# Optimization experiments

Measured on AMD Instinct MI355X. Metric: run time of the kernel, lower is better.

The kernel has to match this reference:

```python
import jax, jax.numpy as jnp
import numpy as np


def setup_inputs() -> dict:
    key = jax.random.key(0)
    k1, k2 = jax.random.split(key)
    z = jax.random.normal(k1, (16, 256, 4096), dtype=jnp.float32)  # (B, z_dim, T)
    embedding = jax.random.normal(k2, (1024, 256), dtype=jnp.float32)  # (z_num, z_dim)
    return {"z": z, "embedding": embedding}


def reference(z, embedding):
    # z: (B, C, T) -> (B, T, C), matching z.transpose(1, 2)
    zt = jnp.transpose(z, (0, 2, 1))
    B, T, C = zt.shape
    z_flat = zt.reshape(-1, C)  # (N, C), N = B*T

    # squared-euclidean distances: ||z||^2 + ||e||^2 - 2 z e^T  -> (N, K)
    distances = (
        jnp.sum(z_flat * z_flat, axis=1, keepdims=True)
        + jnp.sum(embedding * embedding, axis=1)
        - 2.0 * z_flat @ embedding.T
    )
    encoding_idx = jnp.argmin(distances, axis=1)  # (N,)
    z_vq = embedding[encoding_idx].reshape(B, T, C)

    # perplexity of code usage (one-hot scatter -> mean)
    K = embedding.shape[0]
    counts = jnp.zeros((K,), dtype=jnp.float32).at[encoding_idx].add(1.0)
    avg_probs = counts / encoding_idx.shape[0]
    perplexity = jnp.exp(-jnp.sum(avg_probs * jnp.log(avg_probs + 1e-10)))

    # sparsity = cross_entropy(E E^T, arange) = mean(logsumexp(row) - diag)
    logits = embedding @ embedding.T  # (K, K)
    sparsity = jnp.mean(jax.nn.logsumexp(logits, axis=1) - jnp.diag(logits))

    sg = jax.lax.stop_gradient
    z_qut_loss = jnp.sum((z_vq - sg(zt)) ** 2)   # mse_loss reduction='sum'
    z_enc_loss = jnp.sum((sg(z_vq) - zt) ** 2)

    # straight-through estimator
    z_st = zt + sg(z_vq - zt)
    out = jnp.transpose(z_st, (0, 2, 1))  # back to (B, C, T)
    return (out, z_qut_loss, z_enc_loss, perplexity, sparsity)
```

## Files before the change

### kernel.cpp

```cpp
#include <hip/hip_runtime.h>
#include <math.h>

typedef unsigned int u32;
typedef unsigned long long u64;
typedef _Float16 f16x8 __attribute__((ext_vector_type(8)));
typedef _Float16 f16x4 __attribute__((ext_vector_type(4)));
typedef float f32x4 __attribute__((ext_vector_type(4)));
typedef __attribute__((address_space(1))) const char gch;
typedef __attribute__((address_space(3))) char lch;

#define ZD 256
#define KC 1024
#define TT 4096
#define BB 16
#define NROWS (BB*TT)
#define TAU 0.12f
#define FLAGCAP 32768

__device__ __forceinline__ u32 flip32(float s) {
    int i = __float_as_int(s);
    return (u32)(i ^ ((i >> 31) | 0x80000000));
}
__device__ __forceinline__ float unflip32(u32 u) {
    int m = (~(((int)u) >> 31)) | 0x80000000;
    return __int_as_float((int)(u ^ (u32)m));
}

__global__ __launch_bounds__(256)
void vq_prep_kernel(const float* __restrict__ emb, _Float16* __restrict__ eh,
                    float* __restrict__ re, int* __restrict__ cnt) {
    int gid = blockIdx.x * 256 + threadIdx.x;
    if (gid < 2) cnt[gid] = 0;

    int code = gid >> 6;
    int lane = threadIdx.x & 63;
    float4 v = *(const float4*)(emb + (size_t)code * ZD + lane * 4);
    float s = v.x*v.x + v.y*v.y + v.z*v.z + v.w*v.w;
    #pragma unroll
    for (int off = 32; off; off >>= 1) s += __shfl_down(s, off, 64);
    if (lane == 0) re[code] = s;

    f16x4 hv;
    hv[0] = (_Float16)v.x; hv[1] = (_Float16)v.y;
    hv[2] = (_Float16)v.z; hv[3] = (_Float16)v.w;
    *(f16x4*)(eh + (size_t)code * ZD + lane * 4) = hv;
}

__device__ __forceinline__ void stage_half8(const char* ehc, char* dstbase,
                                            int h, int w, int l) {
    const int srow = h * 16384;
    #pragma unroll
    for (int j = 0; j < 2; ++j) {
        const int gi  = w * 2 + j;
        const int c   = 2 * gi + (l >> 5);
        const int kbs = (l & 31) * 16;
        const int off = srow + c * 512 + (kbs ^ ((c & 7) << 4));
        __builtin_amdgcn_global_load_lds((gch*)(ehc + off),
                                         (lch*)(dstbase + gi * 1024), 16, 0, 0);
    }
}

__device__ __forceinline__ void compute_phase16(const char* hb, int h,
                                                const f16x8 (&ah)[8], const float* reL,
                                                float (&v1)[4], float (&v2)[4], int (&i1)[4],
                                                int lane15, int lk) {
    #pragma unroll
    for (int cg = 0; cg < 2; ++cg) {
        const int c  = cg * 16 + lane15;
        const int sw = (lane15 & 7) << 4;
        f16x8 bh[8];
        #pragma unroll
        for (int ks = 0; ks < 8; ++ks)
            bh[ks] = *(const f16x8*)(hb + c * 512 + ((lk * 16 + ks * 64) ^ sw));

        f32x4 ae = {0.f, 0.f, 0.f, 0.f};
        f32x4 ao = {0.f, 0.f, 0.f, 0.f};
        __builtin_amdgcn_s_setprio(1);
        #pragma unroll
        for (int ks = 0; ks < 4; ++ks) {
            ae = __builtin_amdgcn_mfma_f32_16x16x32_f16(ah[2 * ks],     bh[2 * ks],     ae, 0, 0, 0);
            ao = __builtin_amdgcn_mfma_f32_16x16x32_f16(ah[2 * ks + 1], bh[2 * ks + 1], ao, 0, 0, 0);
        }
        __builtin_amdgcn_s_setprio(0);

        const int codeg = h * 32 + c;
        const float rc = reL[codeg];
        #pragma unroll
        for (int r = 0; r < 4; ++r) {
            float s0 = fmaf(-2.f, ae[r] + ao[r], rc);
            float n2 = fminf(fmaxf(v1[r], s0), v2[r]);
            i1[r] = (s0 < v1[r]) ? codeg : i1[r];
            v1[r] = fminf(v1[r], s0);
            v2[r] = n2;
        }
    }
}

__global__ __launch_bounds__(512, 4)
void vq_argmin_mfma(const float* __restrict__ z, const _Float16* __restrict__ eh,
                    const float* __restrict__ emb, const float* __restrict__ re,
                    float* __restrict__ out, float* __restrict__ lossP,
                    int* __restrict__ idx, int* __restrict__ cnt,
                    int* __restrict__ flags) {
    __shared__ __align__(16) char lds[53248];
    float* reL    = (float*)(lds + 49152);
    int*   idsL   = (int*)lds;
    float* wlossL = (float*)(lds + 1024);

    const int tid = threadIdx.x;
    const int w   = tid >> 6;
    const int l   = tid & 63;
    const int lane15 = l & 15;
    const int lk     = l >> 4;
    const int r0  = blockIdx.x * 128;
    const int b   = r0 >> 12;
    const int t0  = r0 & 4095;
    const char* ehc = (const char*)eh;

    *(float2*)(reL + tid * 2) = *(const float2*)(re + tid * 2);

    f16x8 ah[8];
    float zsq = 0.f;
    {
        const char* zb = (const char*)(z + (size_t)b * ZD * TT + t0 + w * 16);
        char* zdst = lds + w * 4096;
        #pragma unroll
        for (int round = 0; round < 4; ++round) {
            #pragma unroll
            for (int j = 0; j < 4; ++j) {
                const int cl = j * 16 + (l >> 2);
                const int tb = (l & 3) * 16;
                const int c  = round * 64 + cl;
                const char* src = zb + (size_t)c * TT * 4 + tb;
                __builtin_amdgcn_global_load_lds((gch*)src, (lch*)(zdst + j * 1024),
                                                 16, 0, 0);
            }
            asm volatile("s_waitcnt vmcnt(0)" ::: "memory");
            __builtin_amdgcn_sched_barrier(0);
            #pragma unroll
            for (int ks2 = 0; ks2 < 2; ++ks2) {
                const int cl0 = ks2 * 32 + lk * 8;
                f16x8 h;
                #pragma unroll
                for (int j = 0; j < 8; ++j) {
                    float v = *(const float*)(zdst + (cl0 + j) * 64 + lane15 * 4);
                    zsq = fmaf(v, v, zsq);
                    h[j] = (_Float16)v;
                }
                ah[round * 2 + ks2] = h;
            }
            asm volatile("s_waitcnt lgkmcnt(0)" ::: "memory");
            __builtin_amdgcn_sched_barrier(0);
        }
    }
    zsq += __shfl_xor(zsq, 16, 64);
    zsq += __shfl_xor(zsq, 32, 64);

    float v1[4], v2[4];
    int   i1[4];
    #pragma unroll
    for (int r = 0; r < 4; ++r) { v1[r] = 3.4e38f; v2[r] = 3.4e38f; i1[r] = 0; }

    asm volatile("s_waitcnt vmcnt(0) lgkmcnt(0)" ::: "memory");
    __syncthreads();
    stage_half8(ehc, lds,         0, w, l);
    stage_half8(ehc, lds + 16384, 1, w, l);

    for (int h = 0; h < 31; ++h) {
        asm volatile("s_waitcnt vmcnt(2)" ::: "memory");
        __builtin_amdgcn_sched_barrier(0);
        __builtin_amdgcn_s_barrier();
        if (h < 30) stage_half8(ehc, lds + ((h + 2) % 3) * 16384, h + 2, w, l);
        compute_phase16(lds + (h % 3) * 16384, h, ah, reL, v1, v2, i1, lane15, lk);
    }
    asm volatile("s_waitcnt vmcnt(0)" ::: "memory");
    __builtin_amdgcn_sched_barrier(0);
    __builtin_amdgcn_s_barrier();
    compute_phase16(lds + (31 % 3) * 16384, 31, ah, reL, v1, v2, i1, lane15, lk);

    #pragma unroll
    for (int off = 1; off < 16; off <<= 1) {
        #pragma unroll
        for (int r = 0; r < 4; ++r) {
            float ov1 = __shfl_xor(v1[r], off, 64);
            int   oi1 = __shfl_xor(i1[r], off, 64);
            float ov2 = __shfl_xor(v2[r], off, 64);
            float nv2 = fminf(fmaxf(v1[r], ov1), fminf(v2[r], ov2));
            if (ov1 < v1[r] || (ov1 == v1[r] && oi1 < i1[r])) { v1[r] = ov1; i1[r] = oi1; }
            v2[r] = nv2;
        }
    }

    float zsr[4];
    #pragma unroll
    for (int r = 0; r < 4; ++r) zsr[r] = __shfl(zsq, lk * 4 + r, 64);

    __syncthreads();
    float lossw = 0.f;
    if (lane15 == 0) {
        #pragma unroll
        for (int r = 0; r < 4; ++r) {
            const int row = w * 16 + lk * 4 + r;
            idsL[row] = i1[r];
            const bool fl = (v2[r] - v1[r] < TAU);
            lossw += fl ? zsr[r] : (zsr[r] + v1[r]);
            if (fl) {
                int p = atomicAdd(cnt, 1);
                if (p < FLAGCAP) flags[p] = (r0 + row) | (i1[r] << 16);
            }
        }
    }
    lossw += __shfl_xor(lossw, 16, 64);
    lossw += __shfl_xor(lossw, 32, 64);
    if (l == 0) wlossL[w] = lossw;
    __syncthreads();

    if (tid < 128) idx[r0 + tid] = idsL[tid];
    if (tid == 0) {
        float s = 0.f;
        #pragma unroll
        for (int j = 0; j < 8; ++j) s += wlossL[j];
        lossP[blockIdx.x] = s;
    }

    {
        const int c0 = w * 32;
        float* ob = out + (size_t)b * ZD * TT + t0;
        #pragma unroll
        for (int half = 0; half < 2; ++half) {
            const int tt = half * 64 + l;
            const int ii = idsL[tt];
            const float4* er4 = (const float4*)(emb + (size_t)ii * ZD + c0);
            #pragma unroll
            for (int c4 = 0; c4 < 8; ++c4) {
                float4 ev = er4[c4];
                float* o0 = ob + (size_t)(c0 + c4 * 4) * TT + tt;
                o0[0]      = ev.x;
                o0[TT]     = ev.y;
                o0[2 * TT] = ev.z;
                o0[3 * TT] = ev.w;
            }
        }
    }
}

__global__ __launch_bounds__(256)
void vq_fixup_spar(const float* __restrict__ z, const float* __restrict__ emb,
                   const float* __restrict__ re, const int* __restrict__ cnt,
                   const int* __restrict__ flags, float* __restrict__ out,
                   int* __restrict__ idx, float* __restrict__ spar,
                   float* __restrict__ addP) {
    const int tid = threadIdx.x;
    const int w   = tid >> 6;
    const int lane = tid & 63;

    if (blockIdx.x >= 128) {
        __shared__ __align__(16) float er[8][260];
        __shared__ float wmaxS[8][4];
        __shared__ float wsumS[8][4];
        __shared__ float shD[8];
        const int bid2 = blockIdx.x - 128;
        const int r0   = bid2 * 8;

        for (int i = tid; i < 8 * 256; i += 256) er[i >> 8][i & 255] = emb[(size_t)r0 * ZD + i];
        __syncthreads();

        float dots[4][8];
        #pragma unroll
        for (int cc = 0; cc < 4; ++cc) {
            const int c = cc * 256 + tid;
            const float4* ec = (const float4*)(emb + (size_t)c * ZD);
            float a[8] = {0.f,0.f,0.f,0.f,0.f,0.f,0.f,0.f};
            for (int k4 = 0; k4 < ZD / 4; ++k4) {
                float4 e4 = ec[k4];
                #pragma unroll
                for (int r = 0; r < 8; ++r) {
                    const float* a4 = &er[r][k4 * 4];
                    a[r] = fmaf(e4.x, a4[0], fmaf(e4.y, a4[1],
                           fmaf(e4.z, a4[2], fmaf(e4.w, a4[3], a[r]))));
                }
            }
            #pragma unroll
            for (int r = 0; r < 8; ++r) dots[cc][r] = a[r];
            const int gr = c - r0;
            if (gr >= 0 && gr < 8) shD[gr] = a[gr];
        }
        #pragma unroll
        for (int r = 0; r < 8; ++r) {
            float m = fmaxf(fmaxf(dots[0][r], dots[1][r]), fmaxf(dots[2][r], dots[3][r]));
            #pragma unroll
            for (int off = 32; off; off >>= 1) m = fmaxf(m, __shfl_xor(m, off, 64));
            if (lane == 0) wmaxS[r][w] = m;
        }
        __syncthreads();
        #pragma unroll
        for (int r = 0; r < 8; ++r) {
            const float M = fmaxf(fmaxf(wmaxS[r][0], wmaxS[r][1]),
                                  fmaxf(wmaxS[r][2], wmaxS[r][3]));
            float se = expf(dots[0][r] - M) + expf(dots[1][r] - M)
                     + expf(dots[2][r] - M) + expf(dots[3][r] - M);
            #pragma unroll
            for (int off = 32; off; off >>= 1) se += __shfl_xor(se, off, 64);
            if (lane == 0) wsumS[r][w] = se;
        }
        __syncthreads();
        if (tid == 0) {
            float acc = 0.f;
            #pragma unroll
            for (int r = 0; r < 8; ++r) {
                const float M = fmaxf(fmaxf(wmaxS[r][0], wmaxS[r][1]),
                                      fmaxf(wmaxS[r][2], wmaxS[r][3]));
                const float S = wsumS[r][0] + wsumS[r][1] + wsumS[r][2] + wsumS[r][3];
                acc += M + logf(S) - shD[r];
            }
            spar[bid2] = acc;
        }
        return;
    }

    __shared__ __align__(16) float zs[8][ZD];
    __shared__ u64 sb[4][8];
    __shared__ int nwS[8];
    __shared__ float addS;
    int n = cnt[0];
    if (n > FLAGCAP) n = FLAGCAP;
    float blkLoss = 0.f;

    for (int base = blockIdx.x * 8; base < n; base += 128 * 8) {
        const int nr = (n - base < 8) ? (n - base) : 8;
        __syncthreads();
        for (int i = tid; i < nr * 256; i += 256) {
            const int r = i >> 8, k = i & 255;
            const int rowg = flags[base + r] & 0xFFFF;
            zs[r][k] = z[(size_t)(rowg >> 12) * ZD * TT + (size_t)k * TT + (rowg & 4095)];
        }
        __syncthreads();

        u64 best[8];
        #pragma unroll
        for (int r = 0; r < 8; ++r) best[r] = 0xFFFFFFFFFFFFFFFFull;

        for (int cc = 0; cc < 4; ++cc) {
            const int c = cc * 256 + tid;
            const float4* ec = (const float4*)(emb + (size_t)c * ZD);
            float a[8] = {0.f,0.f,0.f,0.f,0.f,0.f,0.f,0.f};
            for (int k4 = 0; k4 < ZD / 4; ++k4) {
                float4 e4 = ec[k4];
                #pragma unroll
                for (int r = 0; r < 8; ++r) {
                    const float* a4 = &zs[r][k4 * 4];
                    a[r] = fmaf(e4.x, a4[0], fmaf(e4.y, a4[1],
                           fmaf(e4.z, a4[2], fmaf(e4.w, a4[3], a[r]))));
                }
            }
            const float rc = re[c];
            #pragma unroll
            for (int r = 0; r < 8; ++r) {
                if (r < nr) {
                    float s = fmaf(-2.f, a[r], rc);
                    u64 pk = ((u64)flip32(s) << 32) | (u32)c;
                    if (pk < best[r]) best[r] = pk;
                }
            }
        }
        #pragma unroll
        for (int r = 0; r < 8; ++r) {
            if (r < nr) {
                u64 bv = best[r];
                #pragma unroll
                for (int off = 32; off; off >>= 1) {
                    u64 o = (u64)__shfl_xor((long long)bv, off, 64);
                    if (o < bv) bv = o;
                }
                if (lane == 0) sb[w][r] = bv;
            }
        }
        __syncthreads();
        if (tid == 0) addS = 0.f;
        __syncthreads();
        if (tid < nr) {
            u64 m = sb[0][tid];
            if (sb[1][tid] < m) m = sb[1][tid];
            if (sb[2][tid] < m) m = sb[2][tid];
            if (sb[3][tid] < m) m = sb[3][tid];
            const int nc  = (int)(u32)(m & 0xFFFFFFFFull);
            const float s = unflip32((u32)(m >> 32));
            const int rowg = flags[base + tid] & 0xFFFF;
            const int old  = (flags[base + tid] >> 16) & 1023;
            atomicAdd(&addS, s);
            if (nc != old) { idx[rowg] = nc; nwS[tid] = nc; }
            else nwS[tid] = -1;
        }
        __syncthreads();
        if (tid == 0) blkLoss += addS;
        for (int r = 0; r < nr; ++r) {
            const int nw = nwS[r];
            if (nw >= 0) {
                const int rowg = flags[base + r] & 0xFFFF;
                out[(size_t)(rowg >> 12) * ZD * TT + (size_t)tid * TT + (rowg & 4095)]
                    = emb[(size_t)nw * ZD + tid];
            }
        }
    }
    if (tid == 0) addP[blockIdx.x] = blkLoss;
}

__global__ __launch_bounds__(1024)
void vq_final_kernel(const int* __restrict__ idx, const float* __restrict__ spar,
                     const float* __restrict__ lossP, const float* __restrict__ addP,
                     float* __restrict__ scal) {
    __shared__ int   histL[4][1024];
    __shared__ float red[1024];
    const int tid = threadIdx.x;
    const int g   = tid >> 8;

    histL[0][tid] = 0; histL[1][tid] = 0; histL[2][tid] = 0; histL[3][tid] = 0;
    __syncthreads();
    #pragma unroll 4
    for (int i = 0; i < 64; ++i)
        atomicAdd(&histL[g][idx[i * 1024 + tid]], 1);
    __syncthreads();
    const int hc = histL[0][tid] + histL[1][tid] + histL[2][tid] + histL[3][tid];
    float p = (float)hc * (1.0f / (float)NROWS);
    red[tid] = -p * logf(p + 1e-10f);
    __syncthreads();
    for (int st = 512; st; st >>= 1) {
        if (tid < st) red[tid] += red[tid + st];
        __syncthreads();
    }
    if (tid == 0) scal[2] = expf(red[0]);
    __syncthreads();

    red[tid] = (tid < 512 ? lossP[tid] : 0.f) + ((tid < 128) ? addP[tid] : 0.f);
    __syncthreads();
    for (int st = 512; st; st >>= 1) {
        if (tid < st) red[tid] += red[tid + st];
        __syncthreads();
    }
    if (tid == 0) { scal[0] = red[0]; scal[1] = red[0]; }
    __syncthreads();

    red[tid] = (tid < 128) ? spar[tid] : 0.f;
    __syncthreads();
    for (int st = 512; st; st >>= 1) {
        if (tid < st) red[tid] += red[tid + st];
        __syncthreads();
    }
    if (tid == 0) scal[3] = red[0] * (1.0f / (float)KC);
}

extern "C" void kernel_launch(void* const* d_in, const int* in_sizes, int n_in,
                              void* d_out, int out_size, void* d_ws, size_t ws_size,
                              hipStream_t stream) {
    const float* z   = (const float*)d_in[0];
    const float* emb = (const float*)d_in[1];
    float* out = (float*)d_out;
    const size_t NOUT = (size_t)BB * ZD * TT;
    float* scal = out + NOUT;

    float* re    = (float*)d_ws;
    int*   cnt   = (int*)(re + KC);
    int*   flags = cnt + 4;
    float* spar  = (float*)(flags + FLAGCAP);
    float* lossP = spar + 128;
    float* addP  = lossP + 512;
    int*   idx   = (int*)(addP + 128);
    _Float16* eh = (_Float16*)(idx + NROWS);

    vq_prep_kernel<<<256, 256, 0, stream>>>(emb, eh, re, cnt);
    vq_argmin_mfma<<<NROWS / 128, 512, 0, stream>>>(z, eh, emb, re, out, lossP, idx,
                                                    cnt, flags);
    vq_fixup_spar<<<256, 256, 0, stream>>>(z, emb, re, cnt, flags, out, idx, spar, addP);
    vq_final_kernel<<<1, 1024, 0, stream>>>(idx, spar, lossP, addP, scal);
}
```

Before: 172.0 us.

## Move sparsity logsumexp blocks into argmin kernel and widen fixup grid

The K×K sparsity logsumexp work moves out of the fixup kernel and into extra blocks appended to the main MFMA argmin launch. Those blocks now run 512 threads over two column chunks, so they overlap with argmin work instead of waiting behind it. The fixup kernel becomes a pure recompute kernel with 256 blocks instead of 128, and its partial-loss buffer is widened to match. The extra blocks share the argmin kernel's launch bounds and LDS footprint, which could affect how blocks are scheduled and distributed.

```diff
diff --git a/kernel.cpp b/kernel.cpp
--- a/kernel.cpp
+++ b/kernel.cpp
@@ -101,13 +101,85 @@
                     const float* __restrict__ emb, const float* __restrict__ re,
                     float* __restrict__ out, float* __restrict__ lossP,
                     int* __restrict__ idx, int* __restrict__ cnt,
-                    int* __restrict__ flags) {
+                    int* __restrict__ flags, float* __restrict__ spar) {
     __shared__ __align__(16) char lds[53248];
+
+    const int tid = threadIdx.x;
+
+    if (blockIdx.x >= 512) {
+        float* er    = (float*)lds;
+        float* wmaxS = (float*)(lds + 8320);
+        float* wsumS = wmaxS + 64;
+        float* shD   = wsumS + 64;
+        const int bid2 = blockIdx.x - 512;
+        const int r0s  = bid2 * 8;
+        const int wv = tid >> 6, lane = tid & 63;
+
+        for (int i = tid; i < 8 * 256; i += 512)
+            er[(i >> 8) * 260 + (i & 255)] = emb[(size_t)r0s * ZD + i];
+        __syncthreads();
+
+        float dots[2][8];
+        #pragma unroll
+        for (int cc = 0; cc < 2; ++cc) {
+            const int c = cc * 512 + tid;
+            const float4* ec = (const float4*)(emb + (size_t)c * ZD);
+            float a[8] = {0.f,0.f,0.f,0.f,0.f,0.f,0.f,0.f};
+            #pragma unroll 4
+            for (int k4 = 0; k4 < ZD / 4; ++k4) {
+                float4 e4 = ec[k4];
+                #pragma unroll
+                for (int r = 0; r < 8; ++r) {
+                    const float* a4 = &er[r * 260 + k4 * 4];
+                    a[r] = fmaf(e4.x, a4[0], fmaf(e4.y, a4[1],
+                           fmaf(e4.z, a4[2], fmaf(e4.w, a4[3], a[r]))));
+                }
+            }
+            #pragma unroll
+            for (int r = 0; r < 8; ++r) dots[cc][r] = a[r];
+            const int gr = c - r0s;
+            if (gr >= 0 && gr < 8) shD[gr] = a[gr];
+        }
+        #pragma unroll
+        for (int r = 0; r < 8; ++r) {
+            float m = fmaxf(dots[0][r], dots[1][r]);
+            #pragma unroll
+            for (int off = 32; off; off >>= 1) m = fmaxf(m, __shfl_xor(m, off, 64));
+            if (lane == 0) wmaxS[r * 8 + wv] = m;
+        }
+        __syncthreads();
+        #pragma unroll
+        for (int r = 0; r < 8; ++r) {
+            float M = wmaxS[r * 8];
+            #pragma unroll
+            for (int j = 1; j < 8; ++j) M = fmaxf(M, wmaxS[r * 8 + j]);
+            float se = expf(dots[0][r] - M) + expf(dots[1][r] - M);
+            #pragma unroll
+            for (int off = 32; off; off >>= 1) se += __shfl_xor(se, off, 64);
+            if (lane == 0) wsumS[r * 8 + wv] = se;
+        }
+        __syncthreads();
+        if (tid == 0) {
+            float acc = 0.f;
+            #pragma unroll
+            for (int r = 0; r < 8; ++r) {
+                float M = wmaxS[r * 8];
+                #pragma unroll
+                for (int j = 1; j < 8; ++j) M = fmaxf(M, wmaxS[r * 8 + j]);
+                float S = 0.f;
+                #pragma unroll
+                for (int j = 0; j < 8; ++j) S += wsumS[r * 8 + j];
+                acc += M + logf(S) - shD[r];
+            }
+            spar[bid2] = acc;
+        }
+        return;
+    }
+
     float* reL    = (float*)(lds + 49152);
     int*   idsL   = (int*)lds;
     float* wlossL = (float*)(lds + 1024);
 
-    const int tid = threadIdx.x;
     const int w   = tid >> 6;
     const int l   = tid & 63;
     const int lane15 = l & 15;
@@ -245,105 +317,40 @@
 }
 
 __global__ __launch_bounds__(256)
-void vq_fixup_spar(const float* __restrict__ z, const float* __restrict__ emb,
-                   const float* __restrict__ re, const int* __restrict__ cnt,
-                   const int* __restrict__ flags, float* __restrict__ out,
-                   int* __restrict__ idx, float* __restrict__ spar,
-                   float* __restrict__ addP) {
+void vq_fixup_kernel(const float* __restrict__ z, const float* __restrict__ emb,
+                     const float* __restrict__ re, const int* __restrict__ cnt,
+                     const int* __restrict__ flags, float* __restrict__ out,
+                     int* __restrict__ idx, float* __restrict__ addP) {
+    __shared__ __align__(16) float zs[8][ZD];
+    __shared__ u64 sb[4][8];
+    __shared__ int nwS[8];
+    __shared__ float addS;
     const int tid = threadIdx.x;
     const int w   = tid >> 6;
     const int lane = tid & 63;
-
-    if (blockIdx.x >= 128) {
-        __shared__ __align__(16) float er[8][260];
-        __shared__ float wmaxS[8][4];
-        __shared__ float wsumS[8][4];
-        __shared__ float shD[8];
-        const int bid2 = blockIdx.x - 128;
-        const int r0   = bid2 * 8;
-
-        for (int i = tid; i < 8 * 256; i += 256) er[i >> 8][i & 255] = emb[(size_t)r0 * ZD + i];
-        __syncthreads();
-
-        float dots[4][8];
-        #pragma unroll
+    int n = cnt[0];
+    if (n > FLAGCAP) n = FLAGCAP;
+    float blkLoss = 0.f;
+
+    for (int base = blockIdx.x * 8; base < n; base += 256 * 8) {
+        const int nr = (n - base < 8) ? (n - base) : 8;
+        __syncthreads();
+        for (int i = tid; i < nr * 256; i += 256) {
+            const int r = i >> 8, k = i & 255;
+            const int rowg = flags[base + r] & 0xFFFF;
+            zs[r][k] = z[(size_t)(rowg >> 12) * ZD * TT + (size_t)k * TT + (rowg & 4095)];
+        }
+        __syncthreads();
+
+        u64 best[8];
+        #pragma unroll
+        for (int r = 0; r < 8; ++r) best[r] = 0xFFFFFFFFFFFFFFFFull;
+
         for (int cc = 0; cc < 4; ++cc) {
             const int c = cc * 256 + tid;
             const float4* ec = (const float4*)(emb + (size_t)c * ZD);
             float a[8] = {0.f,0.f,0.f,0.f,0.f,0.f,0.f,0.f};
-            for (int k4 = 0; k4 < ZD / 4; ++k4) {
-                float4 e4 = ec[k4];
-                #pragma unroll
-                for (int r = 0; r < 8; ++r) {
-                    const float* a4 = &er[r][k4 * 4];
-                    a[r] = fmaf(e4.x, a4[0], fmaf(e4.y, a4[1],
-                           fmaf(e4.z, a4[2], fmaf(e4.w, a4[3], a[r]))));
-                }
-            }
-            #pragma unroll
-            for (int r = 0; r < 8; ++r) dots[cc][r] = a[r];
-            const int gr = c - r0;
-            if (gr >= 0 && gr < 8) shD[gr] = a[gr];
-        }
-        #pragma unroll
-        for (int r = 0; r < 8; ++r) {
-            float m = fmaxf(fmaxf(dots[0][r], dots[1][r]), fmaxf(dots[2][r], dots[3][r]));
-            #pragma unroll
-            for (int off = 32; off; off >>= 1) m = fmaxf(m, __shfl_xor(m, off, 64));
-            if (lane == 0) wmaxS[r][w] = m;
-        }
-        __syncthreads();
-        #pragma unroll
-        for (int r = 0; r < 8; ++r) {
-            const float M = fmaxf(fmaxf(wmaxS[r][0], wmaxS[r][1]),
-                                  fmaxf(wmaxS[r][2], wmaxS[r][3]));
-            float se = expf(dots[0][r] - M) + expf(dots[1][r] - M)
-                     + expf(dots[2][r] - M) + expf(dots[3][r] - M);
-            #pragma unroll
-            for (int off = 32; off; off >>= 1) se += __shfl_xor(se, off, 64);
-            if (lane == 0) wsumS[r][w] = se;
-        }
-        __syncthreads();
-        if (tid == 0) {
-            float acc = 0.f;
-            #pragma unroll
-            for (int r = 0; r < 8; ++r) {
-                const float M = fmaxf(fmaxf(wmaxS[r][0], wmaxS[r][1]),
-                                      fmaxf(wmaxS[r][2], wmaxS[r][3]));
-                const float S = wsumS[r][0] + wsumS[r][1] + wsumS[r][2] + wsumS[r][3];
-                acc += M + logf(S) - shD[r];
-            }
-            spar[bid2] = acc;
-        }
-        return;
-    }
-
-    __shared__ __align__(16) float zs[8][ZD];
-    __shared__ u64 sb[4][8];
-    __shared__ int nwS[8];
-    __shared__ float addS;
-    int n = cnt[0];
-    if (n > FLAGCAP) n = FLAGCAP;
-    float blkLoss = 0.f;
-
-    for (int base = blockIdx.x * 8; base < n; base += 128 * 8) {
-        const int nr = (n - base < 8) ? (n - base) : 8;
-        __syncthreads();
-        for (int i = tid; i < nr * 256; i += 256) {
-            const int r = i >> 8, k = i & 255;
-            const int rowg = flags[base + r] & 0xFFFF;
-            zs[r][k] = z[(size_t)(rowg >> 12) * ZD * TT + (size_t)k * TT + (rowg & 4095)];
-        }
-        __syncthreads();
-
-        u64 best[8];
-        #pragma unroll
-        for (int r = 0; r < 8; ++r) best[r] = 0xFFFFFFFFFFFFFFFFull;
-
-        for (int cc = 0; cc < 4; ++cc) {
-            const int c = cc * 256 + tid;
-            const float4* ec = (const float4*)(emb + (size_t)c * ZD);
-            float a[8] = {0.f,0.f,0.f,0.f,0.f,0.f,0.f,0.f};
+            #pragma unroll 4
             for (int k4 = 0; k4 < ZD / 4; ++k4) {
                 float4 e4 = ec[k4];
                 #pragma unroll
@@ -431,7 +438,7 @@
     if (tid == 0) scal[2] = expf(red[0]);
     __syncthreads();
 
-    red[tid] = (tid < 512 ? lossP[tid] : 0.f) + ((tid < 128) ? addP[tid] : 0.f);
+    red[tid] = (tid < 512 ? lossP[tid] : 0.f) + ((tid < 256) ? addP[tid] : 0.f);
     __syncthreads();
     for (int st = 512; st; st >>= 1) {
         if (tid < st) red[tid] += red[tid + st];
@@ -464,12 +471,12 @@
     float* spar  = (float*)(flags + FLAGCAP);
     float* lossP = spar + 128;
     float* addP  = lossP + 512;
-    int*   idx   = (int*)(addP + 128);
+    int*   idx   = (int*)(addP + 256);
     _Float16* eh = (_Float16*)(idx + NROWS);
 
     vq_prep_kernel<<<256, 256, 0, stream>>>(emb, eh, re, cnt);
-    vq_argmin_mfma<<<NROWS / 128, 512, 0, stream>>>(z, eh, emb, re, out, lossP, idx,
-                                                    cnt, flags);
-    vq_fixup_spar<<<256, 256, 0, stream>>>(z, emb, re, cnt, flags, out, idx, spar, addP);
+    vq_argmin_mfma<<<512 + 128, 512, 0, stream>>>(z, eh, emb, re, out, lossP, idx,
+                                                  cnt, flags, spar);
+    vq_fixup_kernel<<<256, 256, 0, stream>>>(z, emb, re, cnt, flags, out, idx, addP);
     vq_final_kernel<<<1, 1024, 0, stream>>>(idx, spar, lossP, addP, scal);
 }
```

New measurement: 204.6 us. 19.0% more time.

## Transpose codebook for coalesced sparsity loads and double fixup block count

Applied to the files above, without the earlier changes.

The prep kernel now also writes a transposed fp32 copy of the embedding, so in the sparsity blocks each thread reads codebook elements with stride KC and neighbouring threads hit contiguous addresses, replacing per-thread strided float4 row reads. The fixup kernel grows from 128 to 256 fixup blocks (grid 384) to spread the flagged-row recompute over more workgroups, and the partial-loss buffer and final reduction are resized to match. Inner loops get unroll-4 pragmas. The cost is an extra 1 MB strided scatter in the prep kernel and more workspace.

```diff
diff --git a/kernel.cpp b/kernel.cpp
--- a/kernel.cpp
+++ b/kernel.cpp
@@ -28,7 +28,8 @@
 
 __global__ __launch_bounds__(256)
 void vq_prep_kernel(const float* __restrict__ emb, _Float16* __restrict__ eh,
-                    float* __restrict__ re, int* __restrict__ cnt) {
+                    float* __restrict__ re, int* __restrict__ cnt,
+                    float* __restrict__ embT) {
     int gid = blockIdx.x * 256 + threadIdx.x;
     if (gid < 2) cnt[gid] = 0;
 
@@ -44,6 +45,12 @@
     hv[0] = (_Float16)v.x; hv[1] = (_Float16)v.y;
     hv[2] = (_Float16)v.z; hv[3] = (_Float16)v.w;
     *(f16x4*)(eh + (size_t)code * ZD + lane * 4) = hv;
+
+    float* etc = embT + code;
+    etc[(size_t)(lane * 4 + 0) * KC] = v.x;
+    etc[(size_t)(lane * 4 + 1) * KC] = v.y;
+    etc[(size_t)(lane * 4 + 2) * KC] = v.z;
+    etc[(size_t)(lane * 4 + 3) * KC] = v.w;
 }
 
 __device__ __forceinline__ void stage_half8(const char* ehc, char* dstbase,
@@ -246,20 +253,20 @@
 
 __global__ __launch_bounds__(256)
 void vq_fixup_spar(const float* __restrict__ z, const float* __restrict__ emb,
-                   const float* __restrict__ re, const int* __restrict__ cnt,
-                   const int* __restrict__ flags, float* __restrict__ out,
-                   int* __restrict__ idx, float* __restrict__ spar,
-                   float* __restrict__ addP) {
+                   const float* __restrict__ embT, const float* __restrict__ re,
+                   const int* __restrict__ cnt, const int* __restrict__ flags,
+                   float* __restrict__ out, int* __restrict__ idx,
+                   float* __restrict__ spar, float* __restrict__ addP) {
     const int tid = threadIdx.x;
     const int w   = tid >> 6;
     const int lane = tid & 63;
 
-    if (blockIdx.x >= 128) {
+    if (blockIdx.x >= 256) {
         __shared__ __align__(16) float er[8][260];
         __shared__ float wmaxS[8][4];
         __shared__ float wsumS[8][4];
         __shared__ float shD[8];
-        const int bid2 = blockIdx.x - 128;
+        const int bid2 = blockIdx.x - 256;
         const int r0   = bid2 * 8;
 
         for (int i = tid; i < 8 * 256; i += 256) er[i >> 8][i & 255] = emb[(size_t)r0 * ZD + i];
@@ -269,15 +276,19 @@
         #pragma unroll
         for (int cc = 0; cc < 4; ++cc) {
             const int c = cc * 256 + tid;
-            const float4* ec = (const float4*)(emb + (size_t)c * ZD);
+            const float* etc = embT + c;
             float a[8] = {0.f,0.f,0.f,0.f,0.f,0.f,0.f,0.f};
+            #pragma unroll 4
             for (int k4 = 0; k4 < ZD / 4; ++k4) {
-                float4 e4 = ec[k4];
+                const float ex = etc[(size_t)(k4 * 4 + 0) * KC];
+                const float ey = etc[(size_t)(k4 * 4 + 1) * KC];
+                const float ez = etc[(size_t)(k4 * 4 + 2) * KC];
+                const float ew = etc[(size_t)(k4 * 4 + 3) * KC];
                 #pragma unroll
                 for (int r = 0; r < 8; ++r) {
                     const float* a4 = &er[r][k4 * 4];
-                    a[r] = fmaf(e4.x, a4[0], fmaf(e4.y, a4[1],
-                           fmaf(e4.z, a4[2], fmaf(e4.w, a4[3], a[r]))));
+                    a[r] = fmaf(ex, a4[0], fmaf(ey, a4[1],
+                           fmaf(ez, a4[2], fmaf(ew, a4[3], a[r]))));
                 }
             }
             #pragma unroll
@@ -326,7 +337,7 @@
     if (n > FLAGCAP) n = FLAGCAP;
     float blkLoss = 0.f;
 
-    for (int base = blockIdx.x * 8; base < n; base += 128 * 8) {
+    for (int base = blockIdx.x * 8; base < n; base += 256 * 8) {
         const int nr = (n - base < 8) ? (n - base) : 8;
         __syncthreads();
         for (int i = tid; i < nr * 256; i += 256) {
@@ -344,6 +355,7 @@
             const int c = cc * 256 + tid;
             const float4* ec = (const float4*)(emb + (size_t)c * ZD);
             float a[8] = {0.f,0.f,0.f,0.f,0.f,0.f,0.f,0.f};
+            #pragma unroll 4
             for (int k4 = 0; k4 < ZD / 4; ++k4) {
                 float4 e4 = ec[k4];
                 #pragma unroll
@@ -431,7 +443,7 @@
     if (tid == 0) scal[2] = expf(red[0]);
     __syncthreads();
 
-    red[tid] = (tid < 512 ? lossP[tid] : 0.f) + ((tid < 128) ? addP[tid] : 0.f);
+    red[tid] = (tid < 512 ? lossP[tid] : 0.f) + ((tid < 256) ? addP[tid] : 0.f);
     __syncthreads();
     for (int st = 512; st; st >>= 1) {
         if (tid < st) red[tid] += red[tid + st];
@@ -464,12 +476,14 @@
     float* spar  = (float*)(flags + FLAGCAP);
     float* lossP = spar + 128;
     float* addP  = lossP + 512;
-    int*   idx   = (int*)(addP + 128);
+    int*   idx   = (int*)(addP + 256);
     _Float16* eh = (_Float16*)(idx + NROWS);
-
-    vq_prep_kernel<<<256, 256, 0, stream>>>(emb, eh, re, cnt);
+    float* embT  = (float*)(eh + (size_t)KC * ZD);
+
+    vq_prep_kernel<<<256, 256, 0, stream>>>(emb, eh, re, cnt, embT);
     vq_argmin_mfma<<<NROWS / 128, 512, 0, stream>>>(z, eh, emb, re, out, lossP, idx,
                                                     cnt, flags);
-    vq_fixup_spar<<<256, 256, 0, stream>>>(z, emb, re, cnt, flags, out, idx, spar, addP);
+    vq_fixup_spar<<<384, 256, 0, stream>>>(z, emb, embT, re, cnt, flags, out, idx,
+                                           spar, addP);
     vq_final_kernel<<<1, 1024, 0, stream>>>(idx, spar, lossP, addP, scal);
 }
```

After: 220.9 us. 1.28x slower.

## Split sparsity logsumexp across column chunks and double fixup blocks

Applied to the files above, without the earlier changes.

The sparsity part of the fixup kernel is split so that each block handles one quarter of the codebook columns for 8 rows. It writes a partial max and sum that the final kernel merges with a log-sum-exp combine, using the precomputed squared norms as the diagonal. The argmin-fixup part now gets 256 blocks instead of 128, so the grid grows from 256 to 768 blocks to spread the tail work over more CUs. Both inner dot loops are also partially unrolled. The cost is extra workspace traffic and a somewhat heavier single-block final kernel.

```diff
diff --git a/kernel.cpp b/kernel.cpp
--- a/kernel.cpp
+++ b/kernel.cpp
@@ -248,46 +248,39 @@
 void vq_fixup_spar(const float* __restrict__ z, const float* __restrict__ emb,
                    const float* __restrict__ re, const int* __restrict__ cnt,
                    const int* __restrict__ flags, float* __restrict__ out,
-                   int* __restrict__ idx, float* __restrict__ spar,
-                   float* __restrict__ addP) {
+                   int* __restrict__ idx, float* __restrict__ sparM,
+                   float* __restrict__ sparS, float* __restrict__ addP) {
     const int tid = threadIdx.x;
     const int w   = tid >> 6;
     const int lane = tid & 63;
 
-    if (blockIdx.x >= 128) {
+    if (blockIdx.x >= 256) {
         __shared__ __align__(16) float er[8][260];
         __shared__ float wmaxS[8][4];
         __shared__ float wsumS[8][4];
-        __shared__ float shD[8];
-        const int bid2 = blockIdx.x - 128;
-        const int r0   = bid2 * 8;
+        const int sb = blockIdx.x - 256;
+        const int r0 = (sb >> 2) * 8;
+        const int ch = sb & 3;
+        const int c  = ch * 256 + tid;
 
         for (int i = tid; i < 8 * 256; i += 256) er[i >> 8][i & 255] = emb[(size_t)r0 * ZD + i];
         __syncthreads();
 
-        float dots[4][8];
-        #pragma unroll
-        for (int cc = 0; cc < 4; ++cc) {
-            const int c = cc * 256 + tid;
-            const float4* ec = (const float4*)(emb + (size_t)c * ZD);
-            float a[8] = {0.f,0.f,0.f,0.f,0.f,0.f,0.f,0.f};
-            for (int k4 = 0; k4 < ZD / 4; ++k4) {
-                float4 e4 = ec[k4];
-                #pragma unroll
-                for (int r = 0; r < 8; ++r) {
-                    const float* a4 = &er[r][k4 * 4];
-                    a[r] = fmaf(e4.x, a4[0], fmaf(e4.y, a4[1],
-                           fmaf(e4.z, a4[2], fmaf(e4.w, a4[3], a[r]))));
-                }
-            }
-            #pragma unroll
-            for (int r = 0; r < 8; ++r) dots[cc][r] = a[r];
-            const int gr = c - r0;
-            if (gr >= 0 && gr < 8) shD[gr] = a[gr];
+        const float4* ec = (const float4*)(emb + (size_t)c * ZD);
+        float a[8] = {0.f,0.f,0.f,0.f,0.f,0.f,0.f,0.f};
+        #pragma unroll 4
+        for (int k4 = 0; k4 < ZD / 4; ++k4) {
+            float4 e4 = ec[k4];
+            #pragma unroll
+            for (int r = 0; r < 8; ++r) {
+                const float* a4 = &er[r][k4 * 4];
+                a[r] = fmaf(e4.x, a4[0], fmaf(e4.y, a4[1],
+                       fmaf(e4.z, a4[2], fmaf(e4.w, a4[3], a[r]))));
+            }
         }
         #pragma unroll
         for (int r = 0; r < 8; ++r) {
-            float m = fmaxf(fmaxf(dots[0][r], dots[1][r]), fmaxf(dots[2][r], dots[3][r]));
+            float m = a[r];
             #pragma unroll
             for (int off = 32; off; off >>= 1) m = fmaxf(m, __shfl_xor(m, off, 64));
             if (lane == 0) wmaxS[r][w] = m;
@@ -297,36 +290,32 @@
         for (int r = 0; r < 8; ++r) {
             const float M = fmaxf(fmaxf(wmaxS[r][0], wmaxS[r][1]),
                                   fmaxf(wmaxS[r][2], wmaxS[r][3]));
-            float se = expf(dots[0][r] - M) + expf(dots[1][r] - M)
-                     + expf(dots[2][r] - M) + expf(dots[3][r] - M);
+            float se = expf(a[r] - M);
             #pragma unroll
             for (int off = 32; off; off >>= 1) se += __shfl_xor(se, off, 64);
             if (lane == 0) wsumS[r][w] = se;
         }
         __syncthreads();
-        if (tid == 0) {
-            float acc = 0.f;
-            #pragma unroll
-            for (int r = 0; r < 8; ++r) {
-                const float M = fmaxf(fmaxf(wmaxS[r][0], wmaxS[r][1]),
-                                      fmaxf(wmaxS[r][2], wmaxS[r][3]));
-                const float S = wsumS[r][0] + wsumS[r][1] + wsumS[r][2] + wsumS[r][3];
-                acc += M + logf(S) - shD[r];
-            }
-            spar[bid2] = acc;
+        if (tid < 8) {
+            const float M = fmaxf(fmaxf(wmaxS[tid][0], wmaxS[tid][1]),
+                                  fmaxf(wmaxS[tid][2], wmaxS[tid][3]));
+            const float S = wsumS[tid][0] + wsumS[tid][1]
+                          + wsumS[tid][2] + wsumS[tid][3];
+            sparM[ch * KC + r0 + tid] = M;
+            sparS[ch * KC + r0 + tid] = S;
         }
         return;
     }
 
     __shared__ __align__(16) float zs[8][ZD];
-    __shared__ u64 sb[4][8];
+    __shared__ u64 sb2[4][8];
     __shared__ int nwS[8];
     __shared__ float addS;
     int n = cnt[0];
     if (n > FLAGCAP) n = FLAGCAP;
     float blkLoss = 0.f;
 
-    for (int base = blockIdx.x * 8; base < n; base += 128 * 8) {
+    for (int base = blockIdx.x * 8; base < n; base += 256 * 8) {
         const int nr = (n - base < 8) ? (n - base) : 8;
         __syncthreads();
         for (int i = tid; i < nr * 256; i += 256) {
@@ -344,6 +333,7 @@
             const int c = cc * 256 + tid;
             const float4* ec = (const float4*)(emb + (size_t)c * ZD);
             float a[8] = {0.f,0.f,0.f,0.f,0.f,0.f,0.f,0.f};
+            #pragma unroll 4
             for (int k4 = 0; k4 < ZD / 4; ++k4) {
                 float4 e4 = ec[k4];
                 #pragma unroll
@@ -372,17 +362,17 @@
                     u64 o = (u64)__shfl_xor((long long)bv, off, 64);
                     if (o < bv) bv = o;
                 }
-                if (lane == 0) sb[w][r] = bv;
+                if (lane == 0) sb2[w][r] = bv;
             }
         }
         __syncthreads();
         if (tid == 0) addS = 0.f;
         __syncthreads();
         if (tid < nr) {
-            u64 m = sb[0][tid];
-            if (sb[1][tid] < m) m = sb[1][tid];
-            if (sb[2][tid] < m) m = sb[2][tid];
-            if (sb[3][tid] < m) m = sb[3][tid];
+            u64 m = sb2[0][tid];
+            if (sb2[1][tid] < m) m = sb2[1][tid];
+            if (sb2[2][tid] < m) m = sb2[2][tid];
+            if (sb2[3][tid] < m) m = sb2[3][tid];
             const int nc  = (int)(u32)(m & 0xFFFFFFFFull);
             const float s = unflip32((u32)(m >> 32));
             const int rowg = flags[base + tid] & 0xFFFF;
@@ -406,7 +396,8 @@
 }
 
 __global__ __launch_bounds__(1024)
-void vq_final_kernel(const int* __restrict__ idx, const float* __restrict__ spar,
+void vq_final_kernel(const int* __restrict__ idx, const float* __restrict__ re,
+                     const float* __restrict__ sparM, const float* __restrict__ sparS,
                      const float* __restrict__ lossP, const float* __restrict__ addP,
                      float* __restrict__ scal) {
     __shared__ int   histL[4][1024];
@@ -431,7 +422,7 @@
     if (tid == 0) scal[2] = expf(red[0]);
     __syncthreads();
 
-    red[tid] = (tid < 512 ? lossP[tid] : 0.f) + ((tid < 128) ? addP[tid] : 0.f);
+    red[tid] = (tid < 512 ? lossP[tid] : 0.f) + ((tid < 256) ? addP[tid] : 0.f);
     __syncthreads();
     for (int st = 512; st; st >>= 1) {
         if (tid < st) red[tid] += red[tid + st];
@@ -440,7 +431,14 @@
     if (tid == 0) { scal[0] = red[0]; scal[1] = red[0]; }
     __syncthreads();
 
-    red[tid] = (tid < 128) ? spar[tid] : 0.f;
+    {
+        const float m0 = sparM[tid], m1 = sparM[KC + tid];
+        const float m2 = sparM[2 * KC + tid], m3 = sparM[3 * KC + tid];
+        const float M = fmaxf(fmaxf(m0, m1), fmaxf(m2, m3));
+        const float S = sparS[tid] * expf(m0 - M) + sparS[KC + tid] * expf(m1 - M)
+                      + sparS[2 * KC + tid] * expf(m2 - M) + sparS[3 * KC + tid] * expf(m3 - M);
+        red[tid] = M + logf(S) - re[tid];
+    }
     __syncthreads();
     for (int st = 512; st; st >>= 1) {
         if (tid < st) red[tid] += red[tid + st];
@@ -461,15 +459,17 @@
     float* re    = (float*)d_ws;
     int*   cnt   = (int*)(re + KC);
     int*   flags = cnt + 4;
-    float* spar  = (float*)(flags + FLAGCAP);
-    float* lossP = spar + 128;
+    float* sparM = (float*)(flags + FLAGCAP);
+    float* sparS = sparM + 4 * KC;
+    float* lossP = sparS + 4 * KC;
     float* addP  = lossP + 512;
-    int*   idx   = (int*)(addP + 128);
+    int*   idx   = (int*)(addP + 256);
     _Float16* eh = (_Float16*)(idx + NROWS);
 
     vq_prep_kernel<<<256, 256, 0, stream>>>(emb, eh, re, cnt);
     vq_argmin_mfma<<<NROWS / 128, 512, 0, stream>>>(z, eh, emb, re, out, lossP, idx,
                                                     cnt, flags);
-    vq_fixup_spar<<<256, 256, 0, stream>>>(z, emb, re, cnt, flags, out, idx, spar, addP);
-    vq_final_kernel<<<1, 1024, 0, stream>>>(idx, spar, lossP, addP, scal);
-}
+    vq_fixup_spar<<<768, 256, 0, stream>>>(z, emb, re, cnt, flags, out, idx,
+                                           sparM, sparS, addP);
+    vq_final_kernel<<<1, 1024, 0, stream>>>(idx, re, sparM, sparS, lossP, addP, scal);
+}
```

After: 177.6 us. 3.2% more time.
